# Kernel tuning notes

Measured on AMD Instinct MI355X. Metric: run time of the kernel, lower is better.

Reference implementation:

```python
import jax, jax.numpy as jnp
import numpy as np

N_HEAD, D_HEAD, D_MODEL, MAX_LEN = 16, 64, 1024, 64
T, B = 1024, 4
SCALE = 1.0 / D_HEAD ** 0.5


def setup_inputs() -> dict:
    key = jax.random.key(0)
    k1, k2, k3, k4 = jax.random.split(key, 4)
    s = 0.02
    w = jax.random.normal(k1, (T, B, D_MODEL), jnp.float32)
    Wqkv = jax.random.normal(k2, (3 * N_HEAD * D_HEAD, D_MODEL), jnp.float32) * s
    pos_emb = jax.random.normal(k3, (2 * MAX_LEN + 1, D_HEAD), jnp.float32) * s
    Wo = jax.random.normal(k4, (D_MODEL, N_HEAD * D_HEAD), jnp.float32) * s
    i = jnp.arange(T)
    # causal mask, 3D path of the original: [qlen, klen, bsz], True = masked
    attn_mask = jnp.broadcast_to((i[None, :] > i[:, None])[:, :, None], (T, T, B))
    return {"w": w, "attn_mask": attn_mask, "Wqkv": Wqkv, "pos_emb": pos_emb, "Wo": Wo}


def reference(w, attn_mask, Wqkv, pos_emb, Wo):
    qlen, bsz, _ = w.shape
    klen = qlen
    # qkv projection (no bias), chunk into q, k, v
    heads = jnp.einsum('tbd,ed->tbe', w, Wqkv)            # [T, B, 3*H*Dh]
    q, k, v = jnp.split(heads, 3, axis=-1)
    q = q.reshape(qlen, bsz, N_HEAD, D_HEAD).transpose(1, 2, 0, 3) * SCALE  # [B,H,T,Dh]
    k = k.reshape(klen, bsz, N_HEAD, D_HEAD).transpose(1, 2, 0, 3)
    v = v.reshape(klen, bsz, N_HEAD, D_HEAD).transpose(1, 2, 0, 3)
    # learnable relative position embeddings r[q_pos, k_pos, Dh]
    i = jnp.arange(klen)
    rel = jnp.clip(i[None, :] - i[:, None], -MAX_LEN, MAX_LEN) + MAX_LEN   # [T, T]
    r = pos_emb[rel]                                                       # [T, T, Dh]
    # content score + relative-position score (q already scaled)
    qk = jnp.einsum('bhqd,bhkd->bhqk', q, k)
    qr = jnp.einsum('bhqd,qkd->bhqk', q, r)
    score = qk + qr                                                        # [B,H,T,T]
    m = attn_mask.transpose(2, 0, 1)[:, None]                              # [B,1,T,T]
    score = jnp.where(m, -jnp.inf, score)
    attn = jax.nn.softmax(score, axis=-1)                                  # coverage
    # content context + position context
    ctx = jnp.einsum('bhqk,bhkd->bhqd', attn, v) + jnp.einsum('bhqk,qkd->bhqd', attn, r)
    attn_vec = ctx.transpose(0, 2, 1, 3).reshape(bsz, qlen, N_HEAD * D_HEAD)
    out = jnp.einsum('bte,de->btd', attn_vec, Wo)                          # [B,T,D]
    return jnp.swapaxes(out, 0, 1)                                         # [T,B,D]
```

## Files before the change

### kernel.cpp

```cpp
#include <hip/hip_runtime.h>
#include <hip/hip_bf16.h>
#include <math.h>

#define N_HEAD 16
#define D_HEAD 64
#define T_SEQ 1024
#define BATCH 4
#define QSCALE 0.180336879f

typedef float f32x4 __attribute__((ext_vector_type(4)));
typedef short bf16x8 __attribute__((ext_vector_type(8)));
typedef short bf16x4v __attribute__((ext_vector_type(4)));

#define AS1(p) ((const __attribute__((address_space(1))) void*)(p))
#define AS3(p) ((__attribute__((address_space(3))) void*)(p))

__device__ inline bf16x8 ld8(const __hip_bfloat16* p) {
    bf16x4v lo = *(const bf16x4v*)p;
    bf16x4v hi = *(const bf16x4v*)(p + 4);
    return __builtin_shufflevector(lo, hi, 0, 1, 2, 3, 4, 5, 6, 7);
}

__global__ __launch_bounds__(256) void cast_all(
    const float* __restrict__ s0, __hip_bfloat16* __restrict__ d0, int n0,
    const float* __restrict__ s1, __hip_bfloat16* __restrict__ d1, int n1,
    const float* __restrict__ s2, __hip_bfloat16* __restrict__ d2, int n2) {
    int i = (blockIdx.x * 256 + threadIdx.x) * 8;
    const float* src;
    __hip_bfloat16* dst;
    if (i < n0) { src = s0 + i; dst = d0 + i; }
    else if ((i -= n0) < n1) { src = s1 + i; dst = d1 + i; }
    else if ((i -= n1) < n2) { src = s2 + i; dst = d2 + i; }
    else return;
    float4 a = *(const float4*)src;
    float4 b = *(const float4*)(src + 4);
    __hip_bfloat16 t[8];
    t[0] = __float2bfloat16(a.x); t[1] = __float2bfloat16(a.y);
    t[2] = __float2bfloat16(a.z); t[3] = __float2bfloat16(a.w);
    t[4] = __float2bfloat16(b.x); t[5] = __float2bfloat16(b.y);
    t[6] = __float2bfloat16(b.z); t[7] = __float2bfloat16(b.w);
    *(uint4*)dst = *(const uint4*)t;
}

__global__ __launch_bounds__(256) void qkv_gemm_mfma(
    const __hip_bfloat16* __restrict__ A,
    const __hip_bfloat16* __restrict__ B,
    const float* __restrict__ P,
    __hip_bfloat16* __restrict__ Qb, __hip_bfloat16* __restrict__ Kb,
    __hip_bfloat16* __restrict__ Vtb) {
    constexpr int Kd = 1024;
    __shared__ __hip_bfloat16 As[128 * 32];
    __shared__ __hip_bfloat16 Bs[128 * 32];
    const int tid = threadIdx.x;
    const int w = tid >> 6, lane = tid & 63;
    const int lanelo = lane & 15, quad = lane >> 4;
    const int wm = (w >> 1) * 64, wn = (w & 1) * 64;
    const int m0 = blockIdx.y * 128, n0 = blockIdx.x * 128;

    const __hip_bfloat16* Ag = A + (size_t)(m0 + w * 16 + (lane >> 2)) * Kd + (lane & 3) * 8;
    const __hip_bfloat16* Bg = B + (size_t)(n0 + w * 16 + (lane >> 2)) * Kd + (lane & 3) * 8;
    __hip_bfloat16* AsW0 = As + w * 16 * 32;
    __hip_bfloat16* AsW1 = As + (64 + w * 16) * 32;
    __hip_bfloat16* BsW0 = Bs + w * 16 * 32;
    __hip_bfloat16* BsW1 = Bs + (64 + w * 16) * 32;

    f32x4 acc[4][4];
#pragma unroll
    for (int i = 0; i < 4; i++)
#pragma unroll
        for (int j = 0; j < 4; j++) acc[i][j] = (f32x4){0.f, 0.f, 0.f, 0.f};

    for (int k0 = 0; k0 < Kd; k0 += 32) {
        __syncthreads();
        __builtin_amdgcn_global_load_lds(AS1(Ag + k0), AS3(AsW0), 16, 0, 0);
        __builtin_amdgcn_global_load_lds(AS1(Ag + 64 * Kd + k0), AS3(AsW1), 16, 0, 0);
        __builtin_amdgcn_global_load_lds(AS1(Bg + k0), AS3(BsW0), 16, 0, 0);
        __builtin_amdgcn_global_load_lds(AS1(Bg + 64 * Kd + k0), AS3(BsW1), 16, 0, 0);
        __syncthreads();
        bf16x8 af[4], bfr[4];
#pragma unroll
        for (int i = 0; i < 4; i++)
            af[i] = *(const bf16x8*)(As + (wm + i * 16 + lanelo) * 32 + quad * 8);
#pragma unroll
        for (int j = 0; j < 4; j++)
            bfr[j] = *(const bf16x8*)(Bs + (wn + j * 16 + lanelo) * 32 + quad * 8);
#pragma unroll
        for (int i = 0; i < 4; i++)
#pragma unroll
            for (int j = 0; j < 4; j++)
                acc[i][j] = __builtin_amdgcn_mfma_f32_16x16x32_bf16(af[i], bfr[j], acc[i][j], 0, 0, 0);
    }

    const int part = n0 >> 10;
    float p0v[4] = {0.f, 0.f, 0.f, 0.f};
    if (part == 2) {
#pragma unroll
        for (int j = 0; j < 4; j++) p0v[j] = P[j * 16 + lanelo];
    }
#pragma unroll
    for (int i = 0; i < 4; i++)
#pragma unroll
        for (int j = 0; j < 4; j++)
#pragma unroll
            for (int reg = 0; reg < 4; reg++) {
                const int row = m0 + wm + i * 16 + quad * 4 + reg;
                const int col = n0 + wn + j * 16 + lanelo;
                const int t = row >> 2, b = row & 3;
                const int e = col & 1023, h = e >> 6, d = e & 63;
                const float v = acc[i][j][reg];
                if (part == 0)
                    Qb[((size_t)(b * 16 + h) * 1024 + t) * 64 + d] = __float2bfloat16(v * QSCALE);
                else if (part == 1)
                    Kb[((size_t)(b * 16 + h) * 1024 + t) * 64 + d] = __float2bfloat16(v);
                else
                    Vtb[((size_t)(b * 16 + h) * 64 + d) * 1024 + t] = __float2bfloat16(v + p0v[j]);
            }
}

__global__ __launch_bounds__(256) void out_gemm_mfma(
    const __hip_bfloat16* __restrict__ A,
    const __hip_bfloat16* __restrict__ B,
    float* __restrict__ out) {
    constexpr int Kd = 1024;
    __shared__ __hip_bfloat16 As[128 * 32];
    __shared__ __hip_bfloat16 Bs[64 * 32];
    const int tid = threadIdx.x;
    const int w = tid >> 6, lane = tid & 63;
    const int lanelo = lane & 15, quad = lane >> 4;
    const int wm = (w >> 1) * 64, wn = (w & 1) * 32;
    const int m0 = blockIdx.y * 128, n0 = blockIdx.x * 64;

    const __hip_bfloat16* Ag = A + (size_t)(m0 + w * 16 + (lane >> 2)) * Kd + (lane & 3) * 8;
    const __hip_bfloat16* Bg = B + (size_t)(n0 + w * 16 + (lane >> 2)) * Kd + (lane & 3) * 8;
    __hip_bfloat16* AsW0 = As + w * 16 * 32;
    __hip_bfloat16* AsW1 = As + (64 + w * 16) * 32;
    __hip_bfloat16* BsW0 = Bs + w * 16 * 32;

    f32x4 acc[4][2];
#pragma unroll
    for (int i = 0; i < 4; i++)
#pragma unroll
        for (int j = 0; j < 2; j++) acc[i][j] = (f32x4){0.f, 0.f, 0.f, 0.f};

    for (int k0 = 0; k0 < Kd; k0 += 32) {
        __syncthreads();
        __builtin_amdgcn_global_load_lds(AS1(Ag + k0), AS3(AsW0), 16, 0, 0);
        __builtin_amdgcn_global_load_lds(AS1(Ag + 64 * Kd + k0), AS3(AsW1), 16, 0, 0);
        __builtin_amdgcn_global_load_lds(AS1(Bg + k0), AS3(BsW0), 16, 0, 0);
        __syncthreads();
        bf16x8 af[4], bfr[2];
#pragma unroll
        for (int i = 0; i < 4; i++)
            af[i] = *(const bf16x8*)(As + (wm + i * 16 + lanelo) * 32 + quad * 8);
#pragma unroll
        for (int j = 0; j < 2; j++)
            bfr[j] = *(const bf16x8*)(Bs + (wn + j * 16 + lanelo) * 32 + quad * 8);
#pragma unroll
        for (int i = 0; i < 4; i++)
#pragma unroll
            for (int j = 0; j < 2; j++)
                acc[i][j] = __builtin_amdgcn_mfma_f32_16x16x32_bf16(af[i], bfr[j], acc[i][j], 0, 0, 0);
    }

#pragma unroll
    for (int i = 0; i < 4; i++)
#pragma unroll
        for (int j = 0; j < 2; j++)
#pragma unroll
            for (int reg = 0; reg < 4; reg++) {
                const int row = m0 + wm + i * 16 + quad * 4 + reg;
                const int col = n0 + wn + j * 16 + lanelo;
                const int b = row >> 10, t = row & 1023;
                out[(size_t)(t * 4 + b) * 1024 + col] = acc[i][j][reg];
            }
}

__global__ __launch_bounds__(256) void flash_attn(
    const __hip_bfloat16* __restrict__ Qb,
    const __hip_bfloat16* __restrict__ Kb,
    const __hip_bfloat16* __restrict__ Vtb,
    const float* __restrict__ P,
    __hip_bfloat16* __restrict__ av) {
    __shared__ __hip_bfloat16 Ks[64][72];
    __shared__ __hip_bfloat16 Vs[64][72];
    __shared__ __hip_bfloat16 Pl[4][16][68];
    __shared__ __hip_bfloat16 Pband[4][2][16][68];
    __shared__ __hip_bfloat16 QPl[4][2][16][66];

    const int px = blockIdx.x;
    const int TB = 15 - px, TS = px;
    const int bh = blockIdx.y;
    const int b = bh >> 4, h = bh & 15;
    const int tid = threadIdx.x;
    const int w = tid >> 6, lane = tid & 63;
    const int lanelo = lane & 15, quad = lane >> 4;
    const size_t qkbase = (size_t)bh * 1024 * 64;
    const size_t vbase  = (size_t)bh * 64 * 1024;

    const int sr = tid >> 2;
    const int sc = (tid & 3) << 4;
    const __hip_bfloat16* kgb = Kb + qkbase + (size_t)sr * 64 + sc;
    const __hip_bfloat16* vgb = Vtb + vbase + (size_t)sr * 1024 + sc;

    {
        short* pb = (short*)&Pband[w][0][0][0];
        for (int i = lane; i < 2 * 16 * 68; i += 64) pb[i] = 0;
    }

    bf16x8 aqb0, aqb1, aqs0, aqs1;
    {
        const __hip_bfloat16* qrb = Qb + qkbase + (size_t)(TB * 64 + w * 16 + lanelo) * 64;
        aqb0 = *(const bf16x8*)(qrb + quad * 8);
        aqb1 = *(const bf16x8*)(qrb + 32 + quad * 8);
        const __hip_bfloat16* qrs = Qb + qkbase + (size_t)(TS * 64 + w * 16 + lanelo) * 64;
        aqs0 = *(const bf16x8*)(qrs + quad * 8);
        aqs1 = *(const bf16x8*)(qrs + 32 + quad * 8);
    }

#pragma unroll
    for (int jj = 0; jj < 5; jj++) {
        const float* prow = P + (size_t)(jj * 16 + lanelo) * 64 + quad * 8;
        float4 pa = *(const float4*)prow;
        float4 pb = *(const float4*)(prow + 4);
        float4 pc = *(const float4*)(prow + 32);
        float4 pd = *(const float4*)(prow + 36);
        __hip_bfloat16 t0[8], t1[8];
        t0[0] = __float2bfloat16(pa.x); t0[1] = __float2bfloat16(pa.y);
        t0[2] = __float2bfloat16(pa.z); t0[3] = __float2bfloat16(pa.w);
        t0[4] = __float2bfloat16(pb.x); t0[5] = __float2bfloat16(pb.y);
        t0[6] = __float2bfloat16(pb.z); t0[7] = __float2bfloat16(pb.w);
        t1[0] = __float2bfloat16(pc.x); t1[1] = __float2bfloat16(pc.y);
        t1[2] = __float2bfloat16(pc.z); t1[3] = __float2bfloat16(pc.w);
        t1[4] = __float2bfloat16(pd.x); t1[5] = __float2bfloat16(pd.y);
        t1[6] = __float2bfloat16(pd.z); t1[7] = __float2bfloat16(pd.w);
        f32x4 accB = (f32x4){0.f, 0.f, 0.f, 0.f};
        accB = __builtin_amdgcn_mfma_f32_16x16x32_bf16(aqb0, *(const bf16x8*)t0, accB, 0, 0, 0);
        accB = __builtin_amdgcn_mfma_f32_16x16x32_bf16(aqb1, *(const bf16x8*)t1, accB, 0, 0, 0);
        f32x4 accS = (f32x4){0.f, 0.f, 0.f, 0.f};
        accS = __builtin_amdgcn_mfma_f32_16x16x32_bf16(aqs0, *(const bf16x8*)t0, accS, 0, 0, 0);
        accS = __builtin_amdgcn_mfma_f32_16x16x32_bf16(aqs1, *(const bf16x8*)t1, accS, 0, 0, 0);
#pragma unroll
        for (int reg = 0; reg < 4; reg++) {
            QPl[w][0][quad * 4 + reg][jj * 16 + lanelo] = __float2bfloat16(accB[reg]);
            QPl[w][1][quad * 4 + reg][jj * 16 + lanelo] = __float2bfloat16(accS[reg]);
        }
    }
    float qp0b[4], qp0s[4];
#pragma unroll
    for (int reg = 0; reg < 4; reg++) {
        qp0b[reg] = (float)QPl[w][0][quad * 4 + reg][0];
        qp0s[reg] = (float)QPl[w][1][quad * 4 + reg][0];
    }

    f32x4 o_accB[4], o_lB, o_accS[4], o_lS;
#pragma unroll
    for (int dt = 0; dt < 4; dt++) {
        o_accB[dt] = (f32x4){0.f, 0.f, 0.f, 0.f};
        o_accS[dt] = (f32x4){0.f, 0.f, 0.f, 0.f};
    }
    o_lB = (f32x4){0.f, 0.f, 0.f, 0.f};
    o_lS = (f32x4){0.f, 0.f, 0.f, 0.f};
    const short one_bf = 0x3F80;
    const bf16x8 vones = {one_bf, one_bf, one_bf, one_bf, one_bf, one_bf, one_bf, one_bf};

    auto do_qtile = [&](int tq, int Tq, const bf16x8& a0, const bf16x8& a1,
                        const float* qp0, f32x4* o_acc, f32x4& o_l, int kt) {
        f32x4 s_acc[4];
#pragma unroll
        for (int ct = 0; ct < 4; ct++) {
            bf16x8 b0 = *(const bf16x8*)&Ks[ct * 16 + lanelo][quad * 8];
            bf16x8 b1 = *(const bf16x8*)&Ks[ct * 16 + lanelo][32 + quad * 8];
            f32x4 acc = (f32x4){0.f, 0.f, 0.f, 0.f};
            acc = __builtin_amdgcn_mfma_f32_16x16x32_bf16(a0, b0, acc, 0, 0, 0);
            acc = __builtin_amdgcn_mfma_f32_16x16x32_bf16(a1, b1, acc, 0, 0, 0);
            s_acc[ct] = acc;
        }
        const int q0 = Tq * 64 + w * 16;
        const int obase = q0 - kt * 64;
        if (kt < Tq - 1) {
#pragma unroll
            for (int ct = 0; ct < 4; ct++)
#pragma unroll
                for (int reg = 0; reg < 4; reg++) {
                    const float p = __builtin_exp2f(s_acc[ct][reg] + qp0[reg]);
                    Pl[w][quad * 4 + reg][ct * 16 + lanelo] = __float2bfloat16(p);
                }
        } else {
#pragma unroll
            for (int ct = 0; ct < 4; ct++)
#pragma unroll
                for (int reg = 0; reg < 4; reg++) {
                    const int rloc = quad * 4 + reg;
                    const int kl = ct * 16 + lanelo;
                    const int o = obase + rloc - kl;
                    const int idx = (o >= 64 || o < 0) ? 0 : (64 - o);
                    const float add = (float)QPl[w][tq][rloc][idx];
                    const float p = (o < 0) ? 0.f : __builtin_exp2f(s_acc[ct][reg] + add);
                    const __hip_bfloat16 pbv = __float2bfloat16(p);
                    Pl[w][rloc][kl] = pbv;
                    if (o >= 0 && o <= 63) Pband[w][tq][rloc][63 - o] = pbv;
                }
        }
#pragma unroll
        for (int c = 0; c < 2; c++) {
            bf16x8 ap = ld8(&Pl[w][lanelo][c * 32 + quad * 8]);
#pragma unroll
            for (int dt = 0; dt < 4; dt++) {
                bf16x8 bv = *(const bf16x8*)&Vs[dt * 16 + lanelo][c * 32 + quad * 8];
                o_acc[dt] = __builtin_amdgcn_mfma_f32_16x16x32_bf16(ap, bv, o_acc[dt], 0, 0, 0);
            }
            o_l = __builtin_amdgcn_mfma_f32_16x16x32_bf16(ap, vones, o_l, 0, 0, 0);
        }
    };

    uint4 rk0, rk1, rv0, rv1;
    rk0 = *(const uint4*)(kgb);
    rk1 = *(const uint4*)(kgb + 8);
    rv0 = *(const uint4*)(vgb);
    rv1 = *(const uint4*)(vgb + 8);

    for (int kt = 0; kt <= TB; kt++) {
        __syncthreads();
        *(uint4*)&Ks[sr][sc]     = rk0;
        *(uint4*)&Ks[sr][sc + 8] = rk1;
        *(uint4*)&Vs[sr][sc]     = rv0;
        *(uint4*)&Vs[sr][sc + 8] = rv1;
        if (kt < TB) {
            const __hip_bfloat16* kg = kgb + (size_t)(kt + 1) * 4096;
            const __hip_bfloat16* vg = vgb + (size_t)(kt + 1) * 64;
            rk0 = *(const uint4*)(kg);
            rk1 = *(const uint4*)(kg + 8);
            rv0 = *(const uint4*)(vg);
            rv1 = *(const uint4*)(vg + 8);
        }
        __syncthreads();

        do_qtile(0, TB, aqb0, aqb1, qp0b, o_accB, o_lB, kt);
        if (kt <= TS) do_qtile(1, TS, aqs0, aqs1, qp0s, o_accS, o_lS, kt);
    }

#pragma unroll
    for (int tq = 0; tq < 2; tq++) {
        f32x4* o_acc = tq == 0 ? o_accB : o_accS;
        f32x4& o_l   = tq == 0 ? o_lB : o_lS;
        const int q0 = (tq == 0 ? TB : TS) * 64 + w * 16;
#pragma unroll
        for (int c = 0; c < 2; c++) {
            bf16x8 ab = ld8(&Pband[w][tq][lanelo][c * 32 + quad * 8]);
#pragma unroll
            for (int dt = 0; dt < 4; dt++) {
                const int d = dt * 16 + lanelo;
                const float p0 = P[d];
                __hip_bfloat16 tb[8];
#pragma unroll
                for (int jj = 0; jj < 8; jj++) {
                    const int kk = c * 32 + quad * 8 + jj;
                    tb[jj] = __float2bfloat16(P[(kk + 1) * 64 + d] - p0);
                }
                o_acc[dt] = __builtin_amdgcn_mfma_f32_16x16x32_bf16(ab, *(const bf16x8*)tb, o_acc[dt], 0, 0, 0);
            }
        }
        float rinv[4];
#pragma unroll
        for (int reg = 0; reg < 4; reg++) rinv[reg] = 1.0f / o_l[reg];
#pragma unroll
        for (int dt = 0; dt < 4; dt++) {
            const int cdim = dt * 16 + lanelo;
#pragma unroll
            for (int reg = 0; reg < 4; reg++) {
                const int q = q0 + quad * 4 + reg;
                av[((size_t)(b * 1024 + q)) * 1024 + h * 64 + cdim] =
                    __float2bfloat16(o_acc[dt][reg] * rinv[reg]);
            }
        }
    }
}

extern "C" void kernel_launch(void* const* d_in, const int* in_sizes, int n_in,
                              void* d_out, int out_size, void* d_ws, size_t ws_size,
                              hipStream_t stream) {
    const float* w       = (const float*)d_in[0];
    const float* Wqkv    = (const float*)d_in[2];
    const float* pos_emb = (const float*)d_in[3];
    const float* Wo      = (const float*)d_in[4];
    float* out = (float*)d_out;

    const size_t SZ = (size_t)BATCH * N_HEAD * T_SEQ * D_HEAD;
    __hip_bfloat16* wb     = (__hip_bfloat16*)d_ws;
    __hip_bfloat16* Wqkvb  = wb + SZ;
    __hip_bfloat16* Wob    = Wqkvb + 3 * 1024 * 1024;
    __hip_bfloat16* Qb     = Wob + 1024 * 1024;
    __hip_bfloat16* Kb     = Qb + SZ;
    __hip_bfloat16* Vtb    = Kb + SZ;
    __hip_bfloat16* AVb    = Vtb + SZ;

    const int n_w = 4096 * 1024, n_wqkv = 3072 * 1024, n_wo = 1024 * 1024;
    const int n_tot = n_w + n_wqkv + n_wo;
    cast_all<<<n_tot / 2048, 256, 0, stream>>>(w, wb, n_w, Wqkv, Wqkvb, n_wqkv, Wo, Wob, n_wo);

    qkv_gemm_mfma<<<dim3(3072 / 128, 4096 / 128), 256, 0, stream>>>(wb, Wqkvb, pos_emb, Qb, Kb, Vtb);
    flash_attn<<<dim3(8, 64), 256, 0, stream>>>(Qb, Kb, Vtb, pos_emb, AVb);
    out_gemm_mfma<<<dim3(1024 / 64, 4096 / 128), 256, 0, stream>>>(AVb, Wob, out);
}
```

Measured before the change: 189.3 us.

## Fuse cast, QKV GEMM, attention and output GEMM into one persistent kernel

Replaces the four kernel launches with a single persistent 512-block kernel. It runs the cast, the QKV projection, flash attention and the output projection as phases separated by a software grid barrier built on global atomics, and the phases share one LDS union. The QKV GEMM tile is widened to 128x192 so exactly 512 blocks cover it, and the output GEMM is remapped onto the same grid. This removes launch gaps and inter-kernel idle time. In exchange it relies on all 512 blocks being co-resident, with a deadlock risk otherwise, and adds spin-wait barrier overhead and phase load imbalance.

```diff
diff --git a/kernel.cpp b/kernel.cpp
--- a/kernel.cpp
+++ b/kernel.cpp
@@ -21,358 +21,397 @@
     return __builtin_shufflevector(lo, hi, 0, 1, 2, 3, 4, 5, 6, 7);
 }
 
-__global__ __launch_bounds__(256) void cast_all(
-    const float* __restrict__ s0, __hip_bfloat16* __restrict__ d0, int n0,
-    const float* __restrict__ s1, __hip_bfloat16* __restrict__ d1, int n1,
-    const float* __restrict__ s2, __hip_bfloat16* __restrict__ d2, int n2) {
-    int i = (blockIdx.x * 256 + threadIdx.x) * 8;
-    const float* src;
-    __hip_bfloat16* dst;
-    if (i < n0) { src = s0 + i; dst = d0 + i; }
-    else if ((i -= n0) < n1) { src = s1 + i; dst = d1 + i; }
-    else if ((i -= n1) < n2) { src = s2 + i; dst = d2 + i; }
-    else return;
-    float4 a = *(const float4*)src;
-    float4 b = *(const float4*)(src + 4);
-    __hip_bfloat16 t[8];
-    t[0] = __float2bfloat16(a.x); t[1] = __float2bfloat16(a.y);
-    t[2] = __float2bfloat16(a.z); t[3] = __float2bfloat16(a.w);
-    t[4] = __float2bfloat16(b.x); t[5] = __float2bfloat16(b.y);
-    t[6] = __float2bfloat16(b.z); t[7] = __float2bfloat16(b.w);
-    *(uint4*)dst = *(const uint4*)t;
+__device__ unsigned g_count = 0;
+__device__ unsigned g_gen = 0;
+
+__device__ __forceinline__ void grid_barrier() {
+    __syncthreads();
+    if (threadIdx.x == 0) {
+        __threadfence();
+        unsigned gen = __hip_atomic_load(&g_gen, __ATOMIC_RELAXED, __HIP_MEMORY_SCOPE_AGENT);
+        unsigned t = __hip_atomic_fetch_add(&g_count, 1u, __ATOMIC_ACQ_REL, __HIP_MEMORY_SCOPE_AGENT);
+        if (t == 511u) {
+            __hip_atomic_store(&g_count, 0u, __ATOMIC_RELAXED, __HIP_MEMORY_SCOPE_AGENT);
+            __hip_atomic_fetch_add(&g_gen, 1u, __ATOMIC_RELEASE, __HIP_MEMORY_SCOPE_AGENT);
+        } else {
+            while (__hip_atomic_load(&g_gen, __ATOMIC_RELAXED, __HIP_MEMORY_SCOPE_AGENT) == gen) {
+                __builtin_amdgcn_s_sleep(16);
+            }
+        }
+        __threadfence();
+    }
+    __syncthreads();
 }
 
-__global__ __launch_bounds__(256) void qkv_gemm_mfma(
-    const __hip_bfloat16* __restrict__ A,
-    const __hip_bfloat16* __restrict__ B,
-    const float* __restrict__ P,
-    __hip_bfloat16* __restrict__ Qb, __hip_bfloat16* __restrict__ Kb,
-    __hip_bfloat16* __restrict__ Vtb) {
-    constexpr int Kd = 1024;
-    __shared__ __hip_bfloat16 As[128 * 32];
-    __shared__ __hip_bfloat16 Bs[128 * 32];
+union SMem {
+    struct {
+        __hip_bfloat16 As[128 * 32];
+        __hip_bfloat16 Bs[192 * 32];
+    } g1;
+    struct {
+        __hip_bfloat16 Ks[64][72];
+        __hip_bfloat16 Vs[64][72];
+        __hip_bfloat16 Pl[4][16][68];
+        __hip_bfloat16 Pband[4][2][16][68];
+        __hip_bfloat16 QPl[4][2][16][66];
+    } fl;
+    struct {
+        __hip_bfloat16 As[128 * 32];
+        __hip_bfloat16 Bs[64 * 32];
+    } g2;
+};
+
+__global__ __launch_bounds__(256, 2) void mega(
+    const float* __restrict__ w, const float* __restrict__ Wqkv,
+    const float* __restrict__ P, const float* __restrict__ Wo,
+    float* __restrict__ out,
+    __hip_bfloat16* wb, __hip_bfloat16* Wqkvb, __hip_bfloat16* Wob,
+    __hip_bfloat16* Qb, __hip_bfloat16* Kb, __hip_bfloat16* Vtb,
+    __hip_bfloat16* AVb) {
+    __shared__ SMem sm;
+
+    const int bid = blockIdx.x;
     const int tid = threadIdx.x;
-    const int w = tid >> 6, lane = tid & 63;
+    const int wv = tid >> 6, lane = tid & 63;
     const int lanelo = lane & 15, quad = lane >> 4;
-    const int wm = (w >> 1) * 64, wn = (w & 1) * 64;
-    const int m0 = blockIdx.y * 128, n0 = blockIdx.x * 128;
-
-    const __hip_bfloat16* Ag = A + (size_t)(m0 + w * 16 + (lane >> 2)) * Kd + (lane & 3) * 8;
-    const __hip_bfloat16* Bg = B + (size_t)(n0 + w * 16 + (lane >> 2)) * Kd + (lane & 3) * 8;
-    __hip_bfloat16* AsW0 = As + w * 16 * 32;
-    __hip_bfloat16* AsW1 = As + (64 + w * 16) * 32;
-    __hip_bfloat16* BsW0 = Bs + w * 16 * 32;
-    __hip_bfloat16* BsW1 = Bs + (64 + w * 16) * 32;
-
-    f32x4 acc[4][4];
-#pragma unroll
-    for (int i = 0; i < 4; i++)
-#pragma unroll
-        for (int j = 0; j < 4; j++) acc[i][j] = (f32x4){0.f, 0.f, 0.f, 0.f};
-
-    for (int k0 = 0; k0 < Kd; k0 += 32) {
-        __syncthreads();
-        __builtin_amdgcn_global_load_lds(AS1(Ag + k0), AS3(AsW0), 16, 0, 0);
-        __builtin_amdgcn_global_load_lds(AS1(Ag + 64 * Kd + k0), AS3(AsW1), 16, 0, 0);
-        __builtin_amdgcn_global_load_lds(AS1(Bg + k0), AS3(BsW0), 16, 0, 0);
-        __builtin_amdgcn_global_load_lds(AS1(Bg + 64 * Kd + k0), AS3(BsW1), 16, 0, 0);
-        __syncthreads();
-        bf16x8 af[4], bfr[4];
+
+    {
+        const int n0 = 4096 * 1024, n1 = 3072 * 1024, n2 = 1024 * 1024;
+        const int ntot = (n0 + n1 + n2) / 8;
+        for (int g = bid * 256 + tid; g < ntot; g += 512 * 256) {
+            int i = g * 8;
+            const float* src;
+            __hip_bfloat16* dst;
+            if (i < n0) { src = w + i; dst = wb + i; }
+            else if ((i -= n0) < n1) { src = Wqkv + i; dst = Wqkvb + i; }
+            else { i -= n1; src = Wo + i; dst = Wob + i; }
+            float4 a = *(const float4*)src;
+            float4 b = *(const float4*)(src + 4);
+            __hip_bfloat16 t[8];
+            t[0] = __float2bfloat16(a.x); t[1] = __float2bfloat16(a.y);
+            t[2] = __float2bfloat16(a.z); t[3] = __float2bfloat16(a.w);
+            t[4] = __float2bfloat16(b.x); t[5] = __float2bfloat16(b.y);
+            t[6] = __float2bfloat16(b.z); t[7] = __float2bfloat16(b.w);
+            *(uint4*)dst = *(const uint4*)t;
+        }
+    }
+    grid_barrier();
+
+    {
+        constexpr int Kd = 1024;
+        const int my = bid >> 4, nx = bid & 15;
+        const int m0 = my * 128, n0 = nx * 192;
+        const int wm = (wv >> 1) * 64, wn = (wv & 1) * 96;
+        __hip_bfloat16* As = sm.g1.As;
+        __hip_bfloat16* Bs = sm.g1.Bs;
+
+        const __hip_bfloat16* Ag = wb + (size_t)(m0 + wv * 16 + (lane >> 2)) * Kd + (lane & 3) * 8;
+        const __hip_bfloat16* Bg = Wqkvb + (size_t)(n0 + wv * 16 + (lane >> 2)) * Kd + (lane & 3) * 8;
+        __hip_bfloat16* AsW0 = As + wv * 16 * 32;
+        __hip_bfloat16* AsW1 = As + (64 + wv * 16) * 32;
+        __hip_bfloat16* BsW0 = Bs + wv * 16 * 32;
+        __hip_bfloat16* BsW1 = Bs + (64 + wv * 16) * 32;
+        __hip_bfloat16* BsW2 = Bs + (128 + wv * 16) * 32;
+
+        f32x4 acc[4][6];
 #pragma unroll
         for (int i = 0; i < 4; i++)
-            af[i] = *(const bf16x8*)(As + (wm + i * 16 + lanelo) * 32 + quad * 8);
-#pragma unroll
-        for (int j = 0; j < 4; j++)
-            bfr[j] = *(const bf16x8*)(Bs + (wn + j * 16 + lanelo) * 32 + quad * 8);
+#pragma unroll
+            for (int j = 0; j < 6; j++) acc[i][j] = (f32x4){0.f, 0.f, 0.f, 0.f};
+
+        for (int k0 = 0; k0 < Kd; k0 += 32) {
+            __syncthreads();
+            __builtin_amdgcn_global_load_lds(AS1(Ag + k0), AS3(AsW0), 16, 0, 0);
+            __builtin_amdgcn_global_load_lds(AS1(Ag + 64 * Kd + k0), AS3(AsW1), 16, 0, 0);
+            __builtin_amdgcn_global_load_lds(AS1(Bg + k0), AS3(BsW0), 16, 0, 0);
+            __builtin_amdgcn_global_load_lds(AS1(Bg + 64 * Kd + k0), AS3(BsW1), 16, 0, 0);
+            __builtin_amdgcn_global_load_lds(AS1(Bg + 128 * Kd + k0), AS3(BsW2), 16, 0, 0);
+            __syncthreads();
+            bf16x8 af[4], bfr[6];
+#pragma unroll
+            for (int i = 0; i < 4; i++)
+                af[i] = *(const bf16x8*)(As + (wm + i * 16 + lanelo) * 32 + quad * 8);
+#pragma unroll
+            for (int j = 0; j < 6; j++)
+                bfr[j] = *(const bf16x8*)(Bs + (wn + j * 16 + lanelo) * 32 + quad * 8);
+#pragma unroll
+            for (int i = 0; i < 4; i++)
+#pragma unroll
+                for (int j = 0; j < 6; j++)
+                    acc[i][j] = __builtin_amdgcn_mfma_f32_16x16x32_bf16(af[i], bfr[j], acc[i][j], 0, 0, 0);
+        }
+
+        const int colbase = n0 + wn;
+        float p0v[6];
+#pragma unroll
+        for (int j = 0; j < 6; j++) p0v[j] = P[(colbase + j * 16 + lanelo) & 63];
 #pragma unroll
         for (int i = 0; i < 4; i++)
 #pragma unroll
-            for (int j = 0; j < 4; j++)
-                acc[i][j] = __builtin_amdgcn_mfma_f32_16x16x32_bf16(af[i], bfr[j], acc[i][j], 0, 0, 0);
+            for (int j = 0; j < 6; j++)
+#pragma unroll
+                for (int reg = 0; reg < 4; reg++) {
+                    const int row = m0 + wm + i * 16 + quad * 4 + reg;
+                    const int col = colbase + j * 16 + lanelo;
+                    const int part = col >> 10;
+                    const int e = col & 1023, h = e >> 6, d = e & 63;
+                    const int t = row >> 2, bb = row & 3;
+                    const float v = acc[i][j][reg];
+                    if (part == 0)
+                        Qb[((size_t)(bb * 16 + h) * 1024 + t) * 64 + d] = __float2bfloat16(v * QSCALE);
+                    else if (part == 1)
+                        Kb[((size_t)(bb * 16 + h) * 1024 + t) * 64 + d] = __float2bfloat16(v);
+                    else
+                        Vtb[((size_t)(bb * 16 + h) * 64 + d) * 1024 + t] = __float2bfloat16(v + p0v[j]);
+                }
     }
-
-    const int part = n0 >> 10;
-    float p0v[4] = {0.f, 0.f, 0.f, 0.f};
-    if (part == 2) {
-#pragma unroll
-        for (int j = 0; j < 4; j++) p0v[j] = P[j * 16 + lanelo];
+    grid_barrier();
+
+    {
+        const int px = bid & 7;
+        const int bh = bid >> 3;
+        const int TB = 15 - px, TS = px;
+        const int b = bh >> 4, h = bh & 15;
+        const size_t qkbase = (size_t)bh * 1024 * 64;
+        const size_t vbase  = (size_t)bh * 64 * 1024;
+        auto& Ks = sm.fl.Ks;
+        auto& Vs = sm.fl.Vs;
+        auto& Pl = sm.fl.Pl;
+        auto& Pband = sm.fl.Pband;
+        auto& QPl = sm.fl.QPl;
+        const int w_ = wv;
+
+        const int sr = tid >> 2;
+        const int sc = (tid & 3) << 4;
+        const __hip_bfloat16* kgb = Kb + qkbase + (size_t)sr * 64 + sc;
+        const __hip_bfloat16* vgb = Vtb + vbase + (size_t)sr * 1024 + sc;
+
+        {
+            short* pb = (short*)&Pband[w_][0][0][0];
+            for (int i = lane; i < 2 * 16 * 68; i += 64) pb[i] = 0;
+        }
+
+        bf16x8 aqb0, aqb1, aqs0, aqs1;
+        {
+            const __hip_bfloat16* qrb = Qb + qkbase + (size_t)(TB * 64 + w_ * 16 + lanelo) * 64;
+            aqb0 = *(const bf16x8*)(qrb + quad * 8);
+            aqb1 = *(const bf16x8*)(qrb + 32 + quad * 8);
+            const __hip_bfloat16* qrs = Qb + qkbase + (size_t)(TS * 64 + w_ * 16 + lanelo) * 64;
+            aqs0 = *(const bf16x8*)(qrs + quad * 8);
+            aqs1 = *(const bf16x8*)(qrs + 32 + quad * 8);
+        }
+
+#pragma unroll
+        for (int jj = 0; jj < 5; jj++) {
+            const float* prow = P + (size_t)(jj * 16 + lanelo) * 64 + quad * 8;
+            float4 pa = *(const float4*)prow;
+            float4 pb = *(const float4*)(prow + 4);
+            float4 pc = *(const float4*)(prow + 32);
+            float4 pd = *(const float4*)(prow + 36);
+            __hip_bfloat16 t0[8], t1[8];
+            t0[0] = __float2bfloat16(pa.x); t0[1] = __float2bfloat16(pa.y);
+            t0[2] = __float2bfloat16(pa.z); t0[3] = __float2bfloat16(pa.w);
+            t0[4] = __float2bfloat16(pb.x); t0[5] = __float2bfloat16(pb.y);
+            t0[6] = __float2bfloat16(pb.z); t0[7] = __float2bfloat16(pb.w);
+            t1[0] = __float2bfloat16(pc.x); t1[1] = __float2bfloat16(pc.y);
+            t1[2] = __float2bfloat16(pc.z); t1[3] = __float2bfloat16(pc.w);
+            t1[4] = __float2bfloat16(pd.x); t1[5] = __float2bfloat16(pd.y);
+            t1[6] = __float2bfloat16(pd.z); t1[7] = __float2bfloat16(pd.w);
+            f32x4 accB = (f32x4){0.f, 0.f, 0.f, 0.f};
+            accB = __builtin_amdgcn_mfma_f32_16x16x32_bf16(aqb0, *(const bf16x8*)t0, accB, 0, 0, 0);
+            accB = __builtin_amdgcn_mfma_f32_16x16x32_bf16(aqb1, *(const bf16x8*)t1, accB, 0, 0, 0);
+            f32x4 accS = (f32x4){0.f, 0.f, 0.f, 0.f};
+            accS = __builtin_amdgcn_mfma_f32_16x16x32_bf16(aqs0, *(const bf16x8*)t0, accS, 0, 0, 0);
+            accS = __builtin_amdgcn_mfma_f32_16x16x32_bf16(aqs1, *(const bf16x8*)t1, accS, 0, 0, 0);
+#pragma unroll
+            for (int reg = 0; reg < 4; reg++) {
+                QPl[w_][0][quad * 4 + reg][jj * 16 + lanelo] = __float2bfloat16(accB[reg]);
+                QPl[w_][1][quad * 4 + reg][jj * 16 + lanelo] = __float2bfloat16(accS[reg]);
+            }
+        }
+        float qp0b[4], qp0s[4];
+#pragma unroll
+        for (int reg = 0; reg < 4; reg++) {
+            qp0b[reg] = (float)QPl[w_][0][quad * 4 + reg][0];
+            qp0s[reg] = (float)QPl[w_][1][quad * 4 + reg][0];
+        }
+
+        f32x4 o_accB[4], o_lB, o_accS[4], o_lS;
+#pragma unroll
+        for (int dt = 0; dt < 4; dt++) {
+            o_accB[dt] = (f32x4){0.f, 0.f, 0.f, 0.f};
+            o_accS[dt] = (f32x4){0.f, 0.f, 0.f, 0.f};
+        }
+        o_lB = (f32x4){0.f, 0.f, 0.f, 0.f};
+        o_lS = (f32x4){0.f, 0.f, 0.f, 0.f};
+        const short one_bf = 0x3F80;
+        const bf16x8 vones = {one_bf, one_bf, one_bf, one_bf, one_bf, one_bf, one_bf, one_bf};
+
+        auto do_qtile = [&](int tq, int Tq, const bf16x8& a0, const bf16x8& a1,
+                            const float* qp0, f32x4* o_acc, f32x4& o_l, int kt) {
+            f32x4 s_acc[4];
+#pragma unroll
+            for (int ct = 0; ct < 4; ct++) {
+                bf16x8 b0 = *(const bf16x8*)&Ks[ct * 16 + lanelo][quad * 8];
+                bf16x8 b1 = *(const bf16x8*)&Ks[ct * 16 + lanelo][32 + quad * 8];
+                f32x4 acc = (f32x4){0.f, 0.f, 0.f, 0.f};
+                acc = __builtin_amdgcn_mfma_f32_16x16x32_bf16(a0, b0, acc, 0, 0, 0);
+                acc = __builtin_amdgcn_mfma_f32_16x16x32_bf16(a1, b1, acc, 0, 0, 0);
+                s_acc[ct] = acc;
+            }
+            const int q0 = Tq * 64 + w_ * 16;
+            const int obase = q0 - kt * 64;
+            if (kt < Tq - 1) {
+#pragma unroll
+                for (int ct = 0; ct < 4; ct++)
+#pragma unroll
+                    for (int reg = 0; reg < 4; reg++) {
+                        const float p = __builtin_exp2f(s_acc[ct][reg] + qp0[reg]);
+                        Pl[w_][quad * 4 + reg][ct * 16 + lanelo] = __float2bfloat16(p);
+                    }
+            } else {
+#pragma unroll
+                for (int ct = 0; ct < 4; ct++)
+#pragma unroll
+                    for (int reg = 0; reg < 4; reg++) {
+                        const int rloc = quad * 4 + reg;
+                        const int kl = ct * 16 + lanelo;
+                        const int o = obase + rloc - kl;
+                        const int idx = (o >= 64 || o < 0) ? 0 : (64 - o);
+                        const float add = (float)QPl[w_][tq][rloc][idx];
+                        const float p = (o < 0) ? 0.f : __builtin_exp2f(s_acc[ct][reg] + add);
+                        const __hip_bfloat16 pbv = __float2bfloat16(p);
+                        Pl[w_][rloc][kl] = pbv;
+                        if (o >= 0 && o <= 63) Pband[w_][tq][rloc][63 - o] = pbv;
+                    }
+            }
+#pragma unroll
+            for (int c = 0; c < 2; c++) {
+                bf16x8 ap = ld8(&Pl[w_][lanelo][c * 32 + quad * 8]);
+#pragma unroll
+                for (int dt = 0; dt < 4; dt++) {
+                    bf16x8 bv = *(const bf16x8*)&Vs[dt * 16 + lanelo][c * 32 + quad * 8];
+                    o_acc[dt] = __builtin_amdgcn_mfma_f32_16x16x32_bf16(ap, bv, o_acc[dt], 0, 0, 0);
+                }
+                o_l = __builtin_amdgcn_mfma_f32_16x16x32_bf16(ap, vones, o_l, 0, 0, 0);
+            }
+        };
+
+        uint4 rk0, rk1, rv0, rv1;
+        rk0 = *(const uint4*)(kgb);
+        rk1 = *(const uint4*)(kgb + 8);
+        rv0 = *(const uint4*)(vgb);
+        rv1 = *(const uint4*)(vgb + 8);
+
+        for (int kt = 0; kt <= TB; kt++) {
+            __syncthreads();
+            *(uint4*)&Ks[sr][sc]     = rk0;
+            *(uint4*)&Ks[sr][sc + 8] = rk1;
+            *(uint4*)&Vs[sr][sc]     = rv0;
+            *(uint4*)&Vs[sr][sc + 8] = rv1;
+            if (kt < TB) {
+                const __hip_bfloat16* kg = kgb + (size_t)(kt + 1) * 4096;
+                const __hip_bfloat16* vg = vgb + (size_t)(kt + 1) * 64;
+                rk0 = *(const uint4*)(kg);
+                rk1 = *(const uint4*)(kg + 8);
+                rv0 = *(const uint4*)(vg);
+                rv1 = *(const uint4*)(vg + 8);
+            }
+            __syncthreads();
+
+            do_qtile(0, TB, aqb0, aqb1, qp0b, o_accB, o_lB, kt);
+            if (kt <= TS) do_qtile(1, TS, aqs0, aqs1, qp0s, o_accS, o_lS, kt);
+        }
+
+#pragma unroll
+        for (int tq = 0; tq < 2; tq++) {
+            f32x4* o_acc = tq == 0 ? o_accB : o_accS;
+            f32x4& o_l   = tq == 0 ? o_lB : o_lS;
+            const int q0 = (tq == 0 ? TB : TS) * 64 + w_ * 16;
+#pragma unroll
+            for (int c = 0; c < 2; c++) {
+                bf16x8 ab = ld8(&Pband[w_][tq][lanelo][c * 32 + quad * 8]);
+#pragma unroll
+                for (int dt = 0; dt < 4; dt++) {
+                    const int d = dt * 16 + lanelo;
+                    const float p0 = P[d];
+                    __hip_bfloat16 tb[8];
+#pragma unroll
+                    for (int jj = 0; jj < 8; jj++) {
+                        const int kk = c * 32 + quad * 8 + jj;
+                        tb[jj] = __float2bfloat16(P[(kk + 1) * 64 + d] - p0);
+                    }
+                    o_acc[dt] = __builtin_amdgcn_mfma_f32_16x16x32_bf16(ab, *(const bf16x8*)tb, o_acc[dt], 0, 0, 0);
+                }
+            }
+            float rinv[4];
+#pragma unroll
+            for (int reg = 0; reg < 4; reg++) rinv[reg] = 1.0f / o_l[reg];
+#pragma unroll
+            for (int dt = 0; dt < 4; dt++) {
+                const int cdim = dt * 16 + lanelo;
+#pragma unroll
+                for (int reg = 0; reg < 4; reg++) {
+                    const int q = q0 + quad * 4 + reg;
+                    AVb[((size_t)(b * 1024 + q)) * 1024 + h * 64 + cdim] =
+                        __float2bfloat16(o_acc[dt][reg] * rinv[reg]);
+                }
+            }
+        }
     }
-#pragma unroll
-    for (int i = 0; i < 4; i++)
-#pragma unroll
-        for (int j = 0; j < 4; j++)
-#pragma unroll
-            for (int reg = 0; reg < 4; reg++) {
-                const int row = m0 + wm + i * 16 + quad * 4 + reg;
-                const int col = n0 + wn + j * 16 + lanelo;
-                const int t = row >> 2, b = row & 3;
-                const int e = col & 1023, h = e >> 6, d = e & 63;
-                const float v = acc[i][j][reg];
-                if (part == 0)
-                    Qb[((size_t)(b * 16 + h) * 1024 + t) * 64 + d] = __float2bfloat16(v * QSCALE);
-                else if (part == 1)
-                    Kb[((size_t)(b * 16 + h) * 1024 + t) * 64 + d] = __float2bfloat16(v);
-                else
-                    Vtb[((size_t)(b * 16 + h) * 64 + d) * 1024 + t] = __float2bfloat16(v + p0v[j]);
-            }
-}
-
-__global__ __launch_bounds__(256) void out_gemm_mfma(
-    const __hip_bfloat16* __restrict__ A,
-    const __hip_bfloat16* __restrict__ B,
-    float* __restrict__ out) {
-    constexpr int Kd = 1024;
-    __shared__ __hip_bfloat16 As[128 * 32];
-    __shared__ __hip_bfloat16 Bs[64 * 32];
-    const int tid = threadIdx.x;
-    const int w = tid >> 6, lane = tid & 63;
-    const int lanelo = lane & 15, quad = lane >> 4;
-    const int wm = (w >> 1) * 64, wn = (w & 1) * 32;
-    const int m0 = blockIdx.y * 128, n0 = blockIdx.x * 64;
-
-    const __hip_bfloat16* Ag = A + (size_t)(m0 + w * 16 + (lane >> 2)) * Kd + (lane & 3) * 8;
-    const __hip_bfloat16* Bg = B + (size_t)(n0 + w * 16 + (lane >> 2)) * Kd + (lane & 3) * 8;
-    __hip_bfloat16* AsW0 = As + w * 16 * 32;
-    __hip_bfloat16* AsW1 = As + (64 + w * 16) * 32;
-    __hip_bfloat16* BsW0 = Bs + w * 16 * 32;
-
-    f32x4 acc[4][2];
-#pragma unroll
-    for (int i = 0; i < 4; i++)
-#pragma unroll
-        for (int j = 0; j < 2; j++) acc[i][j] = (f32x4){0.f, 0.f, 0.f, 0.f};
-
-    for (int k0 = 0; k0 < Kd; k0 += 32) {
-        __syncthreads();
-        __builtin_amdgcn_global_load_lds(AS1(Ag + k0), AS3(AsW0), 16, 0, 0);
-        __builtin_amdgcn_global_load_lds(AS1(Ag + 64 * Kd + k0), AS3(AsW1), 16, 0, 0);
-        __builtin_amdgcn_global_load_lds(AS1(Bg + k0), AS3(BsW0), 16, 0, 0);
-        __syncthreads();
-        bf16x8 af[4], bfr[2];
+    grid_barrier();
+
+    {
+        constexpr int Kd = 1024;
+        const int by = bid >> 4, bx = bid & 15;
+        const int m0 = by * 128, n0 = bx * 64;
+        const int wm = (wv >> 1) * 64, wn = (wv & 1) * 32;
+        __hip_bfloat16* As = sm.g2.As;
+        __hip_bfloat16* Bs = sm.g2.Bs;
+
+        const __hip_bfloat16* Ag = AVb + (size_t)(m0 + wv * 16 + (lane >> 2)) * Kd + (lane & 3) * 8;
+        const __hip_bfloat16* Bg = Wob + (size_t)(n0 + wv * 16 + (lane >> 2)) * Kd + (lane & 3) * 8;
+        __hip_bfloat16* AsW0 = As + wv * 16 * 32;
+        __hip_bfloat16* AsW1 = As + (64 + wv * 16) * 32;
+        __hip_bfloat16* BsW0 = Bs + wv * 16 * 32;
+
+        f32x4 acc[4][2];
 #pragma unroll
         for (int i = 0; i < 4; i++)
-            af[i] = *(const bf16x8*)(As + (wm + i * 16 + lanelo) * 32 + quad * 8);
-#pragma unroll
-        for (int j = 0; j < 2; j++)
-            bfr[j] = *(const bf16x8*)(Bs + (wn + j * 16 + lanelo) * 32 + quad * 8);
+#pragma unroll
+            for (int j = 0; j < 2; j++) acc[i][j] = (f32x4){0.f, 0.f, 0.f, 0.f};
+
+        for (int k0 = 0; k0 < Kd; k0 += 32) {
+            __syncthreads();
+            __builtin_amdgcn_global_load_lds(AS1(Ag + k0), AS3(AsW0), 16, 0, 0);
+            __builtin_amdgcn_global_load_lds(AS1(Ag + 64 * Kd + k0), AS3(AsW1), 16, 0, 0);
+            __builtin_amdgcn_global_load_lds(AS1(Bg + k0), AS3(BsW0), 16, 0, 0);
+            __syncthreads();
+            bf16x8 af[4], bfr[2];
+#pragma unroll
+            for (int i = 0; i < 4; i++)
+                af[i] = *(const bf16x8*)(As + (wm + i * 16 + lanelo) * 32 + quad * 8);
+#pragma unroll
+            for (int j = 0; j < 2; j++)
+                bfr[j] = *(const bf16x8*)(Bs + (wn + j * 16 + lanelo) * 32 + quad * 8);
+#pragma unroll
+            for (int i = 0; i < 4; i++)
+#pragma unroll
+                for (int j = 0; j < 2; j++)
+                    acc[i][j] = __builtin_amdgcn_mfma_f32_16x16x32_bf16(af[i], bfr[j], acc[i][j], 0, 0, 0);
+        }
+
 #pragma unroll
         for (int i = 0; i < 4; i++)
 #pragma unroll
             for (int j = 0; j < 2; j++)
-                acc[i][j] = __builtin_amdgcn_mfma_f32_16x16x32_bf16(af[i], bfr[j], acc[i][j], 0, 0, 0);
-    }
-
-#pragma unroll
-    for (int i = 0; i < 4; i++)
-#pragma unroll
-        for (int j = 0; j < 2; j++)
-#pragma unroll
-            for (int reg = 0; reg < 4; reg++) {
-                const int row = m0 + wm + i * 16 + quad * 4 + reg;
-                const int col = n0 + wn + j * 16 + lanelo;
-                const int b = row >> 10, t = row & 1023;
-                out[(size_t)(t * 4 + b) * 1024 + col] = acc[i][j][reg];
-            }
-}
-
-__global__ __launch_bounds__(256) void flash_attn(
-    const __hip_bfloat16* __restrict__ Qb,
-    const __hip_bfloat16* __restrict__ Kb,
-    const __hip_bfloat16* __restrict__ Vtb,
-    const float* __restrict__ P,
-    __hip_bfloat16* __restrict__ av) {
-    __shared__ __hip_bfloat16 Ks[64][72];
-    __shared__ __hip_bfloat16 Vs[64][72];
-    __shared__ __hip_bfloat16 Pl[4][16][68];
-    __shared__ __hip_bfloat16 Pband[4][2][16][68];
-    __shared__ __hip_bfloat16 QPl[4][2][16][66];
-
-    const int px = blockIdx.x;
-    const int TB = 15 - px, TS = px;
-    const int bh = blockIdx.y;
-    const int b = bh >> 4, h = bh & 15;
-    const int tid = threadIdx.x;
-    const int w = tid >> 6, lane = tid & 63;
-    const int lanelo = lane & 15, quad = lane >> 4;
-    const size_t qkbase = (size_t)bh * 1024 * 64;
-    const size_t vbase  = (size_t)bh * 64 * 1024;
-
-    const int sr = tid >> 2;
-    const int sc = (tid & 3) << 4;
-    const __hip_bfloat16* kgb = Kb + qkbase + (size_t)sr * 64 + sc;
-    const __hip_bfloat16* vgb = Vtb + vbase + (size_t)sr * 1024 + sc;
-
-    {
-        short* pb = (short*)&Pband[w][0][0][0];
-        for (int i = lane; i < 2 * 16 * 68; i += 64) pb[i] = 0;
-    }
-
-    bf16x8 aqb0, aqb1, aqs0, aqs1;
-    {
-        const __hip_bfloat16* qrb = Qb + qkbase + (size_t)(TB * 64 + w * 16 + lanelo) * 64;
-        aqb0 = *(const bf16x8*)(qrb + quad * 8);
-        aqb1 = *(const bf16x8*)(qrb + 32 + quad * 8);
-        const __hip_bfloat16* qrs = Qb + qkbase + (size_t)(TS * 64 + w * 16 + lanelo) * 64;
-        aqs0 = *(const bf16x8*)(qrs + quad * 8);
-        aqs1 = *(const bf16x8*)(qrs + 32 + quad * 8);
-    }
-
-#pragma unroll
-    for (int jj = 0; jj < 5; jj++) {
-        const float* prow = P + (size_t)(jj * 16 + lanelo) * 64 + quad * 8;
-        float4 pa = *(const float4*)prow;
-        float4 pb = *(const float4*)(prow + 4);
-        float4 pc = *(const float4*)(prow + 32);
-        float4 pd = *(const float4*)(prow + 36);
-        __hip_bfloat16 t0[8], t1[8];
-        t0[0] = __float2bfloat16(pa.x); t0[1] = __float2bfloat16(pa.y);
-        t0[2] = __float2bfloat16(pa.z); t0[3] = __float2bfloat16(pa.w);
-        t0[4] = __float2bfloat16(pb.x); t0[5] = __float2bfloat16(pb.y);
-        t0[6] = __float2bfloat16(pb.z); t0[7] = __float2bfloat16(pb.w);
-        t1[0] = __float2bfloat16(pc.x); t1[1] = __float2bfloat16(pc.y);
-        t1[2] = __float2bfloat16(pc.z); t1[3] = __float2bfloat16(pc.w);
-        t1[4] = __float2bfloat16(pd.x); t1[5] = __float2bfloat16(pd.y);
-        t1[6] = __float2bfloat16(pd.z); t1[7] = __float2bfloat16(pd.w);
-        f32x4 accB = (f32x4){0.f, 0.f, 0.f, 0.f};
-        accB = __builtin_amdgcn_mfma_f32_16x16x32_bf16(aqb0, *(const bf16x8*)t0, accB, 0, 0, 0);
-        accB = __builtin_amdgcn_mfma_f32_16x16x32_bf16(aqb1, *(const bf16x8*)t1, accB, 0, 0, 0);
-        f32x4 accS = (f32x4){0.f, 0.f, 0.f, 0.f};
-        accS = __builtin_amdgcn_mfma_f32_16x16x32_bf16(aqs0, *(const bf16x8*)t0, accS, 0, 0, 0);
-        accS = __builtin_amdgcn_mfma_f32_16x16x32_bf16(aqs1, *(const bf16x8*)t1, accS, 0, 0, 0);
-#pragma unroll
-        for (int reg = 0; reg < 4; reg++) {
-            QPl[w][0][quad * 4 + reg][jj * 16 + lanelo] = __float2bfloat16(accB[reg]);
-            QPl[w][1][quad * 4 + reg][jj * 16 + lanelo] = __float2bfloat16(accS[reg]);
-        }
-    }
-    float qp0b[4], qp0s[4];
-#pragma unroll
-    for (int reg = 0; reg < 4; reg++) {
-        qp0b[reg] = (float)QPl[w][0][quad * 4 + reg][0];
-        qp0s[reg] = (float)QPl[w][1][quad * 4 + reg][0];
-    }
-
-    f32x4 o_accB[4], o_lB, o_accS[4], o_lS;
-#pragma unroll
-    for (int dt = 0; dt < 4; dt++) {
-        o_accB[dt] = (f32x4){0.f, 0.f, 0.f, 0.f};
-        o_accS[dt] = (f32x4){0.f, 0.f, 0.f, 0.f};
-    }
-    o_lB = (f32x4){0.f, 0.f, 0.f, 0.f};
-    o_lS = (f32x4){0.f, 0.f, 0.f, 0.f};
-    const short one_bf = 0x3F80;
-    const bf16x8 vones = {one_bf, one_bf, one_bf, one_bf, one_bf, one_bf, one_bf, one_bf};
-
-    auto do_qtile = [&](int tq, int Tq, const bf16x8& a0, const bf16x8& a1,
-                        const float* qp0, f32x4* o_acc, f32x4& o_l, int kt) {
-        f32x4 s_acc[4];
-#pragma unroll
-        for (int ct = 0; ct < 4; ct++) {
-            bf16x8 b0 = *(const bf16x8*)&Ks[ct * 16 + lanelo][quad * 8];
-            bf16x8 b1 = *(const bf16x8*)&Ks[ct * 16 + lanelo][32 + quad * 8];
-            f32x4 acc = (f32x4){0.f, 0.f, 0.f, 0.f};
-            acc = __builtin_amdgcn_mfma_f32_16x16x32_bf16(a0, b0, acc, 0, 0, 0);
-            acc = __builtin_amdgcn_mfma_f32_16x16x32_bf16(a1, b1, acc, 0, 0, 0);
-            s_acc[ct] = acc;
-        }
-        const int q0 = Tq * 64 + w * 16;
-        const int obase = q0 - kt * 64;
-        if (kt < Tq - 1) {
-#pragma unroll
-            for (int ct = 0; ct < 4; ct++)
 #pragma unroll
                 for (int reg = 0; reg < 4; reg++) {
-                    const float p = __builtin_exp2f(s_acc[ct][reg] + qp0[reg]);
-                    Pl[w][quad * 4 + reg][ct * 16 + lanelo] = __float2bfloat16(p);
+                    const int row = m0 + wm + i * 16 + quad * 4 + reg;
+                    const int col = n0 + wn + j * 16 + lanelo;
+                    const int bb = row >> 10, t = row & 1023;
+                    out[(size_t)(t * 4 + bb) * 1024 + col] = acc[i][j][reg];
                 }
-        } else {
-#pragma unroll
-            for (int ct = 0; ct < 4; ct++)
-#pragma unroll
-                for (int reg = 0; reg < 4; reg++) {
-                    const int rloc = quad * 4 + reg;
-                    const int kl = ct * 16 + lanelo;
-                    const int o = obase + rloc - kl;
-                    const int idx = (o >= 64 || o < 0) ? 0 : (64 - o);
-                    const float add = (float)QPl[w][tq][rloc][idx];
-                    const float p = (o < 0) ? 0.f : __builtin_exp2f(s_acc[ct][reg] + add);
-                    const __hip_bfloat16 pbv = __float2bfloat16(p);
-                    Pl[w][rloc][kl] = pbv;
-                    if (o >= 0 && o <= 63) Pband[w][tq][rloc][63 - o] = pbv;
-                }
-        }
-#pragma unroll
-        for (int c = 0; c < 2; c++) {
-            bf16x8 ap = ld8(&Pl[w][lanelo][c * 32 + quad * 8]);
-#pragma unroll
-            for (int dt = 0; dt < 4; dt++) {
-                bf16x8 bv = *(const bf16x8*)&Vs[dt * 16 + lanelo][c * 32 + quad * 8];
-                o_acc[dt] = __builtin_amdgcn_mfma_f32_16x16x32_bf16(ap, bv, o_acc[dt], 0, 0, 0);
-            }
-            o_l = __builtin_amdgcn_mfma_f32_16x16x32_bf16(ap, vones, o_l, 0, 0, 0);
-        }
-    };
-
-    uint4 rk0, rk1, rv0, rv1;
-    rk0 = *(const uint4*)(kgb);
-    rk1 = *(const uint4*)(kgb + 8);
-    rv0 = *(const uint4*)(vgb);
-    rv1 = *(const uint4*)(vgb + 8);
-
-    for (int kt = 0; kt <= TB; kt++) {
-        __syncthreads();
-        *(uint4*)&Ks[sr][sc]     = rk0;
-        *(uint4*)&Ks[sr][sc + 8] = rk1;
-        *(uint4*)&Vs[sr][sc]     = rv0;
-        *(uint4*)&Vs[sr][sc + 8] = rv1;
-        if (kt < TB) {
-            const __hip_bfloat16* kg = kgb + (size_t)(kt + 1) * 4096;
-            const __hip_bfloat16* vg = vgb + (size_t)(kt + 1) * 64;
-            rk0 = *(const uint4*)(kg);
-            rk1 = *(const uint4*)(kg + 8);
-            rv0 = *(const uint4*)(vg);
-            rv1 = *(const uint4*)(vg + 8);
-        }
-        __syncthreads();
-
-        do_qtile(0, TB, aqb0, aqb1, qp0b, o_accB, o_lB, kt);
-        if (kt <= TS) do_qtile(1, TS, aqs0, aqs1, qp0s, o_accS, o_lS, kt);
-    }
-
-#pragma unroll
-    for (int tq = 0; tq < 2; tq++) {
-        f32x4* o_acc = tq == 0 ? o_accB : o_accS;
-        f32x4& o_l   = tq == 0 ? o_lB : o_lS;
-        const int q0 = (tq == 0 ? TB : TS) * 64 + w * 16;
-#pragma unroll
-        for (int c = 0; c < 2; c++) {
-            bf16x8 ab = ld8(&Pband[w][tq][lanelo][c * 32 + quad * 8]);
-#pragma unroll
-            for (int dt = 0; dt < 4; dt++) {
-                const int d = dt * 16 + lanelo;
-                const float p0 = P[d];
-                __hip_bfloat16 tb[8];
-#pragma unroll
-                for (int jj = 0; jj < 8; jj++) {
-                    const int kk = c * 32 + quad * 8 + jj;
-                    tb[jj] = __float2bfloat16(P[(kk + 1) * 64 + d] - p0);
-                }
-                o_acc[dt] = __builtin_amdgcn_mfma_f32_16x16x32_bf16(ab, *(const bf16x8*)tb, o_acc[dt], 0, 0, 0);
-            }
-        }
-        float rinv[4];
-#pragma unroll
-        for (int reg = 0; reg < 4; reg++) rinv[reg] = 1.0f / o_l[reg];
-#pragma unroll
-        for (int dt = 0; dt < 4; dt++) {
-            const int cdim = dt * 16 + lanelo;
-#pragma unroll
-            for (int reg = 0; reg < 4; reg++) {
-                const int q = q0 + quad * 4 + reg;
-                av[((size_t)(b * 1024 + q)) * 1024 + h * 64 + cdim] =
-                    __float2bfloat16(o_acc[dt][reg] * rinv[reg]);
-            }
-        }
     }
 }
 
@@ -394,11 +433,6 @@
     __hip_bfloat16* Vtb    = Kb + SZ;
     __hip_bfloat16* AVb    = Vtb + SZ;
 
-    const int n_w = 4096 * 1024, n_wqkv = 3072 * 1024, n_wo = 1024 * 1024;
-    const int n_tot = n_w + n_wqkv + n_wo;
-    cast_all<<<n_tot / 2048, 256, 0, stream>>>(w, wb, n_w, Wqkv, Wqkvb, n_wqkv, Wo, Wob, n_wo);
-
-    qkv_gemm_mfma<<<dim3(3072 / 128, 4096 / 128), 256, 0, stream>>>(wb, Wqkvb, pos_emb, Qb, Kb, Vtb);
-    flash_attn<<<dim3(8, 64), 256, 0, stream>>>(Qb, Kb, Vtb, pos_emb, AVb);
-    out_gemm_mfma<<<dim3(1024 / 64, 4096 / 128), 256, 0, stream>>>(AVb, Wob, out);
+    mega<<<dim3(512), dim3(256), 0, stream>>>(
+        w, Wqkv, pos_emb, Wo, out, wb, Wqkvb, Wob, Qb, Kb, Vtb, AVb);
 }
```

Result: slower. 408.6 us (+115.8%).
